# Optimization experiments

Measured on AMD Instinct MI355X. Metric: run time of the kernel, lower is better.

The kernel has to match this reference:

```python
import jax, jax.numpy as jnp
import numpy as np

B, S, H, NH = 2, 2048, 1024, 16
DH = H // NH
FF = 4 * H
EPS = 1e-5


def setup_inputs() -> dict:
    key = jax.random.key(0)
    ks = jax.random.split(key, 16)
    sd = 0.02
    inp = {
        "x": jax.random.normal(ks[0], (B, S, H), dtype=jnp.float32),
        "Wq": jax.random.normal(ks[1], (H, H), dtype=jnp.float32) * sd,
        "bq": jnp.zeros((H,), jnp.float32),
        "Wk": jax.random.normal(ks[2], (H, H), dtype=jnp.float32) * sd,
        "bk": jnp.zeros((H,), jnp.float32),
        "Wv": jax.random.normal(ks[3], (H, H), dtype=jnp.float32) * sd,
        "bv": jnp.zeros((H,), jnp.float32),
        "Wo": jax.random.normal(ks[4], (H, H), dtype=jnp.float32) * sd,
        "bo": jnp.zeros((H,), jnp.float32),
        "W1": jax.random.normal(ks[5], (H, FF), dtype=jnp.float32) * sd,
        "b1": jnp.zeros((FF,), jnp.float32),
        "W2": jax.random.normal(ks[6], (FF, H), dtype=jnp.float32) * sd,
        "b2": jnp.zeros((H,), jnp.float32),
        "g1": jnp.ones((H,), jnp.float32),
        "be1": jnp.zeros((H,), jnp.float32),
        "g2": jnp.ones((H,), jnp.float32),
        "be2": jnp.zeros((H,), jnp.float32),
    }
    return inp


def _layernorm(x, g, b):
    mu = jnp.mean(x, axis=-1, keepdims=True)
    var = jnp.mean(jnp.square(x - mu), axis=-1, keepdims=True)
    return (x - mu) * jax.lax.rsqrt(var + EPS) * g + b


def _block(x, Wq, bq, Wk, bk, Wv, bv, Wo, bo, W1, b1, W2, b2, g1, be1, g2, be2):
    # pre-LN attention
    h = _layernorm(x, g1, be1)
    q = (h @ Wq + bq).reshape(B, S, NH, DH)
    k = (h @ Wk + bk).reshape(B, S, NH, DH)
    v = (h @ Wv + bv).reshape(B, S, NH, DH)
    scale = DH ** -0.5
    scores = jnp.einsum("bqhd,bkhd->bhqk", q, k) * scale  # [B,NH,S,S]
    causal = jnp.tril(jnp.ones((S, S), dtype=bool))
    scores = jnp.where(causal, scores, -jnp.inf)
    attn = jax.nn.softmax(scores, axis=-1)
    out = jnp.einsum("bhqk,bkhd->bqhd", attn, v).reshape(B, S, H)
    x = x + (out @ Wo + bo)
    # pre-LN FFN with exact GELU (torch nn.GELU default)
    h = _layernorm(x, g2, be2)
    h = jax.nn.gelu(h @ W1 + b1, approximate=False)
    return x + (h @ W2 + b2)


def reference(x, Wq, bq, Wk, bk, Wv, bv, Wo, bo, W1, b1, W2, b2, g1, be1, g2, be2):
    return _block(x, Wq, bq, Wk, bk, Wv, bv, Wo, bo, W1, b1, W2, b2, g1, be1, g2, be2)
```

## Files before the change

kernel.cpp:

```cpp
#include <hip/hip_runtime.h>
#include <cstdint>
#include <cstddef>

typedef unsigned short u16;
typedef __attribute__((ext_vector_type(8))) __bf16 bf16v8;
typedef __attribute__((ext_vector_type(8))) unsigned short u16x8;
typedef __attribute__((ext_vector_type(4))) float f32x4;

constexpr int Bc = 2, Sc = 2048, Hc = 1024, NHc = 16, DHc = 64, FFc = 4096;
constexpr int Mc = Bc * Sc;

__device__ __forceinline__ u16 f2bf(float f) {
  unsigned u = __builtin_bit_cast(unsigned, f);
  return (u16)((u + 0x7FFFu + ((u >> 16) & 1u)) >> 16);
}

__device__ __forceinline__ int xcd_swz(int bid, int n) {
  const int q = n >> 3;
  return (bid & 7) * q + (bid >> 3);
}

__device__ __forceinline__ void gload_lds16(const void* g, void* l) {
  __builtin_amdgcn_global_load_lds(
      (const __attribute__((address_space(1))) unsigned*)(uintptr_t)g,
      (__attribute__((address_space(3))) unsigned*)(unsigned)(uintptr_t)l,
      16, 0, 0);
}

struct WP6 { const float* wq; const float* wk; const float* wv; const float* wo;
             const float* w1; const float* w2; };
__global__ __launch_bounds__(256) void wconv_all_kernel(WP6 p, u16* __restrict__ wqkv,
                                                        u16* __restrict__ d1,
                                                        u16* __restrict__ d2) {
  __shared__ float tile[64][65];
  const int z = blockIdx.z;
  const int bid = blockIdx.x;
  const float* W;
  u16* dst;
  int K, N;
  if (z < 4) {
    if (bid >= 256) return;
    W = (z == 0) ? p.wq : (z == 1) ? p.wk : (z == 2) ? p.wv : p.wo;
    dst = wqkv + ((size_t)z << 20);
    K = 1024; N = 1024;
  } else if (z == 4) {
    W = p.w1; dst = d1; K = 1024; N = 4096;
  } else {
    W = p.w2; dst = d2; K = 4096; N = 1024;
  }
  const int nb = N >> 6;
  const int n0 = (bid % nb) << 6, k0 = (bid / nb) << 6;
  const int t = threadIdx.x;
  const int col = t & 63, r0 = t >> 6;
#pragma unroll
  for (int i = 0; i < 16; ++i) {
    int r = (i << 2) + r0;
    tile[r][col] = W[(size_t)(k0 + r) * N + n0 + col];
  }
  __syncthreads();
#pragma unroll
  for (int i = 0; i < 16; ++i) {
    int n = (i << 2) + r0;
    dst[(size_t)(n0 + n) * K + k0 + col] = f2bf(tile[col][n]);
  }
}

__global__ __launch_bounds__(256) void ln_kernel(const float* __restrict__ x,
                                                 const float* __restrict__ g,
                                                 const float* __restrict__ be,
                                                 u16* __restrict__ y) {
  const int row = blockIdx.x;
  const int t = threadIdx.x;
  const float4 v = ((const float4*)(x + (size_t)row * Hc))[t];
  float s1 = v.x + v.y + v.z + v.w;
  float s2 = v.x * v.x + v.y * v.y + v.z * v.z + v.w * v.w;
#pragma unroll
  for (int o = 32; o > 0; o >>= 1) {
    s1 += __shfl_xor(s1, o);
    s2 += __shfl_xor(s2, o);
  }
  __shared__ float r1[4], r2[4];
  const int wave = t >> 6, lane = t & 63;
  if (lane == 0) { r1[wave] = s1; r2[wave] = s2; }
  __syncthreads();
  s1 = r1[0] + r1[1] + r1[2] + r1[3];
  s2 = r2[0] + r2[1] + r2[2] + r2[3];
  const float mu = s1 * (1.f / Hc);
  const float var = s2 * (1.f / Hc) - mu * mu;
  const float rs = rsqrtf(var + 1e-5f);
  const float4 gv = ((const float4*)g)[t];
  const float4 bv = ((const float4*)be)[t];
  ushort4 ov;
  ov.x = f2bf((v.x - mu) * rs * gv.x + bv.x);
  ov.y = f2bf((v.y - mu) * rs * gv.y + bv.y);
  ov.z = f2bf((v.z - mu) * rs * gv.z + bv.z);
  ov.w = f2bf((v.w - mu) * rs * gv.w + bv.w);
  ((ushort4*)(y + (size_t)row * Hc))[t] = ov;
}

template <int EPI>
__global__ __launch_bounds__(256, 2) void gemm_kernel(
    const u16* __restrict__ A, const u16* __restrict__ Bt,
    const float* __restrict__ bias, const float* __restrict__ res,
    u16* __restrict__ outb, float* __restrict__ outf,
    int N, int Kext, int lda, int ldb, int nx) {
  __shared__ __align__(16) char smraw[32768];
  u16 (*As)[128][32] = (u16(*)[128][32])smraw;
  u16 (*Bs)[128][32] = (u16(*)[128][32])(smraw + 16384);
  float (*Cs)[16][132] = (float(*)[16][132])smraw;

  const int t = threadIdx.x;
  const int wave = t >> 6, lane = t & 63;
  const int pid = xcd_swz(blockIdx.x, gridDim.x);
  const int bn = pid % nx, bm = pid / nx;
  const int wm = wave >> 1, wn = wave & 1;
  const int fr = lane & 15, fk = (lane >> 4) << 3;

  f32x4 acc[4][4] = {};

  const int srow = (wave << 4) + (lane >> 2);
  const int scol = (lane & 3) << 3;
  const u16* Ag0 = A + (size_t)(bm * 128 + srow) * lda + scol;
  const u16* Ag1 = Ag0 + (size_t)64 * lda;
  const u16* Bg0 = Bt + (size_t)(bn * 128 + srow) * ldb + scol;
  const u16* Bg1 = Bg0 + (size_t)64 * ldb;

  const int nk = Kext >> 5;
  auto STAGE = [&](int buf, int k0) {
    gload_lds16(Ag0 + k0, &As[buf][wave << 4][0]);
    gload_lds16(Ag1 + k0, &As[buf][64 + (wave << 4)][0]);
    gload_lds16(Bg0 + k0, &Bs[buf][wave << 4][0]);
    gload_lds16(Bg1 + k0, &Bs[buf][64 + (wave << 4)][0]);
  };

  STAGE(0, 0);
  int cur = 0;
  for (int kt = 0; kt < nk; ++kt) {
    if (kt + 1 < nk) {
      STAGE(cur ^ 1, (kt + 1) << 5);
      asm volatile("s_waitcnt vmcnt(4)" ::: "memory");
    } else {
      asm volatile("s_waitcnt vmcnt(0)" ::: "memory");
    }
    __builtin_amdgcn_s_barrier();
    bf16v8 af[4], bfr[4];
#pragma unroll
    for (int i = 0; i < 4; ++i) af[i] = *(const bf16v8*)&As[cur][(wm << 6) + (i << 4) + fr][fk];
#pragma unroll
    for (int j = 0; j < 4; ++j) bfr[j] = *(const bf16v8*)&Bs[cur][(wn << 6) + (j << 4) + fr][fk];
    asm volatile("s_waitcnt lgkmcnt(0)" ::: "memory");
    __builtin_amdgcn_s_barrier();
    __builtin_amdgcn_s_setprio(1);
#pragma unroll
    for (int i = 0; i < 4; ++i)
#pragma unroll
      for (int j = 0; j < 4; ++j)
        acc[i][j] = __builtin_amdgcn_mfma_f32_16x16x32_bf16(af[i], bfr[j], acc[i][j], 0, 0, 0);
    __builtin_amdgcn_s_setprio(0);
    cur ^= 1;
  }
  __syncthreads();

  const int cr = (lane >> 4) << 2, cc = lane & 15;
  const int b2 = t >> 7, u = t & 127, lr = u >> 3, c0 = (u & 7) << 4;

  for (int i = 0; i < 4; ++i) {
#pragma unroll
    for (int j = 0; j < 4; ++j) {
      int col = (wn << 6) + (j << 4) + cc;
      float bz = bias[(bn << 7) + col];
#pragma unroll
      for (int r = 0; r < 4; ++r) Cs[wm][cr + r][col] = acc[i][j][r] + bz;
    }
    __syncthreads();
    {
      const float* crow = &Cs[b2][lr][c0];
      f32x4 v0 = *(const f32x4*)(crow);
      f32x4 v1 = *(const f32x4*)(crow + 4);
      f32x4 v2 = *(const f32x4*)(crow + 8);
      f32x4 v3 = *(const f32x4*)(crow + 12);
      const int grow = (bm << 7) + (b2 << 6) + (i << 4) + lr;
      const int gc = (bn << 7) + c0;
      const size_t base = (size_t)grow * N + gc;
      if constexpr (EPI == 0 || EPI == 1) {
        float vv[16];
#pragma unroll
        for (int k = 0; k < 4; ++k) { vv[k] = v0[k]; vv[4 + k] = v1[k]; vv[8 + k] = v2[k]; vv[12 + k] = v3[k]; }
        if constexpr (EPI == 1) {
#pragma unroll
          for (int k = 0; k < 16; ++k)
            vv[k] = 0.5f * vv[k] * (1.0f + erff(vv[k] * 0.70710678118654752f));
        }
        u16x8 o0, o1;
#pragma unroll
        for (int k = 0; k < 8; ++k) { o0[k] = f2bf(vv[k]); o1[k] = f2bf(vv[8 + k]); }
        *(u16x8*)&outb[base] = o0;
        *(u16x8*)&outb[base + 8] = o1;
      } else {
        const f32x4* rp = (const f32x4*)&res[base];
        v0 += rp[0]; v1 += rp[1]; v2 += rp[2]; v3 += rp[3];
        f32x4* op = (f32x4*)&outf[base];
        op[0] = v0; op[1] = v1; op[2] = v2; op[3] = v3;
      }
    }
    __syncthreads();
  }
}

template <int EPI>
__global__ __launch_bounds__(256, 2) void gemm_p_kernel(
    const u16* __restrict__ A, const u16* __restrict__ Bt,
    const float* __restrict__ bias, const float* __restrict__ res,
    u16* __restrict__ outb, float* __restrict__ outf,
    int N, int Kext, int lda, int ldb, int nx) {
  __shared__ __align__(16) char smraw[49152];
  u16 (*As)[128][32] = (u16(*)[128][32])smraw;
  u16 (*Bs)[128][32] = (u16(*)[128][32])(smraw + 24576);
  float (*Cs)[16][132] = (float(*)[16][132])smraw;

  const int t = threadIdx.x;
  const int wave = t >> 6, lane = t & 63;
  const int pid = xcd_swz(blockIdx.x, gridDim.x);
  const int bn = pid % nx, bm = pid / nx;
  const int wm = wave >> 1, wn = wave & 1;
  const int fr = lane & 15, fk = (lane >> 4) << 3;

  f32x4 acc[4][4] = {};

  const int srow = (wave << 4) + (lane >> 2);
  const int scol = (lane & 3) << 3;
  const u16* Ag0 = A + (size_t)(bm * 128 + srow) * lda + scol;
  const u16* Ag1 = Ag0 + (size_t)64 * lda;
  const u16* Bg0 = Bt + (size_t)(bn * 128 + srow) * ldb + scol;
  const u16* Bg1 = Bg0 + (size_t)64 * ldb;

  const int nk = Kext >> 5;
  auto STAGE = [&](int buf, int k0) {
    gload_lds16(Ag0 + k0, &As[buf][wave << 4][0]);
    gload_lds16(Ag1 + k0, &As[buf][64 + (wave << 4)][0]);
    gload_lds16(Bg0 + k0, &Bs[buf][wave << 4][0]);
    gload_lds16(Bg1 + k0, &Bs[buf][64 + (wave << 4)][0]);
  };

  STAGE(0, 0);
  STAGE(1, 32);
  int cur = 0;
  for (int kt = 0; kt < nk; ++kt) {
    if (kt + 2 < nk) {
      int sb = cur + 2; if (sb >= 3) sb -= 3;
      STAGE(sb, (kt + 2) << 5);
      asm volatile("s_waitcnt vmcnt(8)" ::: "memory");
    } else if (kt + 1 < nk) {
      asm volatile("s_waitcnt vmcnt(4)" ::: "memory");
    } else {
      asm volatile("s_waitcnt vmcnt(0)" ::: "memory");
    }
    __builtin_amdgcn_s_barrier();
    bf16v8 af[4], bfr[4];
#pragma unroll
    for (int i = 0; i < 4; ++i) af[i] = *(const bf16v8*)&As[cur][(wm << 6) + (i << 4) + fr][fk];
#pragma unroll
    for (int j = 0; j < 4; ++j) bfr[j] = *(const bf16v8*)&Bs[cur][(wn << 6) + (j << 4) + fr][fk];
    asm volatile("s_waitcnt lgkmcnt(0)" ::: "memory");
    __builtin_amdgcn_s_barrier();
    __builtin_amdgcn_s_setprio(1);
#pragma unroll
    for (int i = 0; i < 4; ++i)
#pragma unroll
      for (int j = 0; j < 4; ++j)
        acc[i][j] = __builtin_amdgcn_mfma_f32_16x16x32_bf16(af[i], bfr[j], acc[i][j], 0, 0, 0);
    __builtin_amdgcn_s_setprio(0);
    cur = (cur + 1 == 3) ? 0 : cur + 1;
  }
  __syncthreads();

  const int cr = (lane >> 4) << 2, cc = lane & 15;
  const int b2 = t >> 7, u = t & 127, lr = u >> 3, c0 = (u & 7) << 4;

  for (int i = 0; i < 4; ++i) {
#pragma unroll
    for (int j = 0; j < 4; ++j) {
      int col = (wn << 6) + (j << 4) + cc;
      float bz = bias[(bn << 7) + col];
#pragma unroll
      for (int r = 0; r < 4; ++r) Cs[wm][cr + r][col] = acc[i][j][r] + bz;
    }
    __syncthreads();
    {
      const float* crow = &Cs[b2][lr][c0];
      f32x4 v0 = *(const f32x4*)(crow);
      f32x4 v1 = *(const f32x4*)(crow + 4);
      f32x4 v2 = *(const f32x4*)(crow + 8);
      f32x4 v3 = *(const f32x4*)(crow + 12);
      const int grow = (bm << 7) + (b2 << 6) + (i << 4) + lr;
      const int gc = (bn << 7) + c0;
      const size_t base = (size_t)grow * N + gc;
      if constexpr (EPI == 0 || EPI == 1) {
        float vv[16];
#pragma unroll
        for (int k = 0; k < 4; ++k) { vv[k] = v0[k]; vv[4 + k] = v1[k]; vv[8 + k] = v2[k]; vv[12 + k] = v3[k]; }
        if constexpr (EPI == 1) {
#pragma unroll
          for (int k = 0; k < 16; ++k)
            vv[k] = 0.5f * vv[k] * (1.0f + erff(vv[k] * 0.70710678118654752f));
        }
        u16x8 o0, o1;
#pragma unroll
        for (int k = 0; k < 8; ++k) { o0[k] = f2bf(vv[k]); o1[k] = f2bf(vv[8 + k]); }
        *(u16x8*)&outb[base] = o0;
        *(u16x8*)&outb[base + 8] = o1;
      } else {
        const f32x4* rp = (const f32x4*)&res[base];
        v0 += rp[0]; v1 += rp[1]; v2 += rp[2]; v3 += rp[3];
        f32x4* op = (f32x4*)&outf[base];
        op[0] = v0; op[1] = v1; op[2] = v2; op[3] = v3;
      }
    }
    __syncthreads();
  }
}

__global__ __launch_bounds__(256, 2) void qkv_gemm_kernel(
    const u16* __restrict__ A, const u16* __restrict__ Bt,
    const float* __restrict__ bq, const float* __restrict__ bk,
    const float* __restrict__ bv,
    u16* __restrict__ Qb, u16* __restrict__ Kb, u16* __restrict__ Vtg) {
  constexpr int K = 1024;
  __shared__ __align__(16) char smraw[49152];
  u16 (*As)[128][32] = (u16(*)[128][32])smraw;
  u16 (*Bs)[128][32] = (u16(*)[128][32])(smraw + 24576);
  float (*Cs)[16][132] = (float(*)[16][132])smraw;

  const int t = threadIdx.x;
  const int wave = t >> 6, lane = t & 63;
  const int pid = xcd_swz(blockIdx.x, 768);
  const int bn = pid % 24, bm = pid / 24;
  const int wm = wave >> 1, wn = wave & 1;
  const int fr = lane & 15, fk = (lane >> 4) << 3;
  const int seg = bn >> 3;

  f32x4 acc[4][4] = {};

  const int srow = (wave << 4) + (lane >> 2);
  const int scol = (lane & 3) << 3;
  const u16* Ag0 = A + (size_t)(bm * 128 + srow) * K + scol;
  const u16* Ag1 = Ag0 + (size_t)64 * K;
  const u16* Bg0 = Bt + (size_t)(bn * 128 + srow) * K + scol;
  const u16* Bg1 = Bg0 + (size_t)64 * K;

  const int nk = K >> 5;
  auto STAGE = [&](int buf, int k0) {
    gload_lds16(Ag0 + k0, &As[buf][wave << 4][0]);
    gload_lds16(Ag1 + k0, &As[buf][64 + (wave << 4)][0]);
    gload_lds16(Bg0 + k0, &Bs[buf][wave << 4][0]);
    gload_lds16(Bg1 + k0, &Bs[buf][64 + (wave << 4)][0]);
  };

  STAGE(0, 0);
  STAGE(1, 32);
  int cur = 0;
  for (int kt = 0; kt < nk; ++kt) {
    if (kt + 2 < nk) {
      int sb = cur + 2; if (sb >= 3) sb -= 3;
      STAGE(sb, (kt + 2) << 5);
      asm volatile("s_waitcnt vmcnt(8)" ::: "memory");
    } else if (kt + 1 < nk) {
      asm volatile("s_waitcnt vmcnt(4)" ::: "memory");
    } else {
      asm volatile("s_waitcnt vmcnt(0)" ::: "memory");
    }
    __builtin_amdgcn_s_barrier();
    bf16v8 af[4], bfr[4];
#pragma unroll
    for (int i = 0; i < 4; ++i) af[i] = *(const bf16v8*)&As[cur][(wm << 6) + (i << 4) + fr][fk];
#pragma unroll
    for (int j = 0; j < 4; ++j) bfr[j] = *(const bf16v8*)&Bs[cur][(wn << 6) + (j << 4) + fr][fk];
    asm volatile("s_waitcnt lgkmcnt(0)" ::: "memory");
    __builtin_amdgcn_s_barrier();
    __builtin_amdgcn_s_setprio(1);
#pragma unroll
    for (int i = 0; i < 4; ++i)
#pragma unroll
      for (int j = 0; j < 4; ++j)
        acc[i][j] = __builtin_amdgcn_mfma_f32_16x16x32_bf16(af[i], bfr[j], acc[i][j], 0, 0, 0);
    __builtin_amdgcn_s_setprio(0);
    cur = (cur + 1 == 3) ? 0 : cur + 1;
  }
  __syncthreads();

  const int cr = (lane >> 4) << 2, cc = lane & 15;
  const int b2 = t >> 7, u = t & 127, lr = u >> 3, c0 = (u & 7) << 4;
  const float* bp = (seg == 0) ? bq : (seg == 1) ? bk : bv;

  for (int i = 0; i < 4; ++i) {
#pragma unroll
    for (int j = 0; j < 4; ++j) {
      int col = (wn << 6) + (j << 4) + cc;
      float bz = bp[((bn << 7) + col) & 1023];
#pragma unroll
      for (int r = 0; r < 4; ++r) Cs[wm][cr + r][col] = acc[i][j][r] + bz;
    }
    __syncthreads();
    if (seg < 2) {
      const float* crow = &Cs[b2][lr][c0];
      f32x4 v0 = *(const f32x4*)(crow);
      f32x4 v1 = *(const f32x4*)(crow + 4);
      f32x4 v2 = *(const f32x4*)(crow + 8);
      f32x4 v3 = *(const f32x4*)(crow + 12);
      const int grow = (bm << 7) + (b2 << 6) + (i << 4) + lr;
      const int cn0 = (((bn & 7) << 7) + c0);
      u16* dst = (seg == 0) ? Qb : Kb;
      u16x8 o0, o1;
#pragma unroll
      for (int k = 0; k < 4; ++k) {
        o0[k] = f2bf(v0[k]); o0[4 + k] = f2bf(v1[k]);
        o1[k] = f2bf(v2[k]); o1[4 + k] = f2bf(v3[k]);
      }
      *(u16x8*)&dst[(size_t)grow * 1024 + cn0] = o0;
      *(u16x8*)&dst[(size_t)grow * 1024 + cn0 + 8] = o1;
    } else {
      const int cv = ((bn & 7) << 7) + u;
      const int h = cv >> 6, dh = cv & 63;
#pragma unroll
      for (int oct = 0; oct < 2; ++oct) {
        u16x8 o;
#pragma unroll
        for (int k = 0; k < 8; ++k) o[k] = f2bf(Cs[b2][(oct << 3) + k][u]);
        const int srow2 = (bm << 7) + (b2 << 6) + (i << 4) + (oct << 3);
        const int bb = srow2 >> 11, s = srow2 & 2047;
        size_t idx = ((size_t)(bb * 16 + h)) * (64 * 2048) + (size_t)dh * 2048 + s;
        *(u16x8*)&Vtg[idx] = o;
      }
    }
    __syncthreads();
  }
}

__global__ __launch_bounds__(512, 2) void attn_kernel(const u16* __restrict__ Q,
                                                      const u16* __restrict__ Kb,
                                                      const u16* __restrict__ Vt,
                                                      u16* __restrict__ O) {
  constexpr float CS = 0.18033688011112042f;
  constexpr float M2 = 8.0f;
  const int pid = xcd_swz(blockIdx.x, 256);
  const int bx = pid & 7, bh = pid >> 3;
  const int t = threadIdx.x, wave = t >> 6, lane = t & 63;
  const int fr = lane & 15, fk = (lane >> 4) << 3;

  __shared__ u16 Ks[2][64][72];
  __shared__ u16 Vs[2][64][72];
  __shared__ u16 Ps[8][16][72];

  const size_t base = ((size_t)(bh >> 4) * Sc) * Hc + (bh & 15) * DHc;
  const u16* Qp = Q + base;
  const u16* Kp = Kb + base;
  const u16* Vp = Vt + (size_t)bh * (64 * 2048);

  const int r_st = t >> 3;
  const int co_st = (t & 7) << 3;

  bf16v8 ones;
#pragma unroll
  for (int k = 0; k < 8; ++k) ones[k] = (__bf16)1.0f;

  for (int half = 0; half < 2; ++half) {
    const int QT = half ? (15 - bx) : bx;
    const int q0 = QT << 7;
    const int nt = (QT + 1) << 1;

    const int qrow = q0 + (wave << 4) + fr;
    const bf16v8 qf0 = *(const bf16v8*)&Qp[(size_t)qrow * Hc + fk];
    const bf16v8 qf1 = *(const bf16v8*)&Qp[(size_t)qrow * Hc + 32 + fk];

    f32x4 oacc[4] = {};
    f32x4 osum = {};

    const int crow0 = q0 + (wave << 4) + ((lane >> 4) << 2);

    u16x8 rk, rv;
    auto LD = [&](int kv0) {
      rk = *(const u16x8*)&Kp[(size_t)(kv0 + r_st) * Hc + co_st];
      rv = *(const u16x8*)&Vp[(size_t)r_st * 2048 + kv0 + co_st];
    };
    auto WR = [&](int buf) {
      *(u16x8*)&Ks[buf][r_st][co_st] = rk;
      *(u16x8*)&Vs[buf][r_st][co_st] = rv;
    };

    LD(0);
    WR(0);
    __syncthreads();
    int cur = 0;
    for (int it = 0; it < nt; ++it) {
      const int kv0 = it << 6;
      const bool hasnext = (it + 1 < nt);
      if (hasnext) LD(kv0 + 64);

      f32x4 sc[4];
      __builtin_amdgcn_s_setprio(1);
#pragma unroll
      for (int c = 0; c < 4; ++c) {
        bf16v8 kf0 = *(const bf16v8*)&Ks[cur][(c << 4) + fr][fk];
        bf16v8 kf1 = *(const bf16v8*)&Ks[cur][(c << 4) + fr][32 + fk];
        f32x4 a = {0.f, 0.f, 0.f, 0.f};
        a = __builtin_amdgcn_mfma_f32_16x16x32_bf16(qf0, kf0, a, 0, 0, 0);
        a = __builtin_amdgcn_mfma_f32_16x16x32_bf16(qf1, kf1, a, 0, 0, 0);
        sc[c] = a;
      }
      __builtin_amdgcn_s_setprio(0);

      if (kv0 + 64 > q0) {
#pragma unroll
        for (int c = 0; c < 4; ++c)
#pragma unroll
          for (int r = 0; r < 4; ++r) {
            int kv = kv0 + (c << 4) + fr;
            if (kv > crow0 + r) sc[c][r] = -INFINITY;
          }
      }

#pragma unroll
      for (int c = 0; c < 4; ++c)
#pragma unroll
        for (int r = 0; r < 4; ++r) {
          float p = exp2f(fmaf(sc[c][r], CS, -M2));
          Ps[wave][((lane >> 4) << 2) + r][(c << 4) + fr] = f2bf(p);
        }

      const bf16v8 pa0 = *(const bf16v8*)&Ps[wave][fr][fk];
      const bf16v8 pa1 = *(const bf16v8*)&Ps[wave][fr][32 + fk];
      __builtin_amdgcn_s_setprio(1);
#pragma unroll
      for (int f = 0; f < 4; ++f) {
        bf16v8 vf0 = *(const bf16v8*)&Vs[cur][(f << 4) + fr][fk];
        bf16v8 vf1 = *(const bf16v8*)&Vs[cur][(f << 4) + fr][32 + fk];
        oacc[f] = __builtin_amdgcn_mfma_f32_16x16x32_bf16(pa0, vf0, oacc[f], 0, 0, 0);
        oacc[f] = __builtin_amdgcn_mfma_f32_16x16x32_bf16(pa1, vf1, oacc[f], 0, 0, 0);
      }
      osum = __builtin_amdgcn_mfma_f32_16x16x32_bf16(pa0, ones, osum, 0, 0, 0);
      osum = __builtin_amdgcn_mfma_f32_16x16x32_bf16(pa1, ones, osum, 0, 0, 0);
      __builtin_amdgcn_s_setprio(0);

      if (hasnext) WR(cur ^ 1);
      __syncthreads();
      cur ^= 1;
    }
#pragma unroll
    for (int r = 0; r < 4; ++r) {
      float inv = 1.0f / osum[r];
      int row = crow0 + r;
#pragma unroll
      for (int f = 0; f < 4; ++f)
        O[base + (size_t)row * Hc + (f << 4) + fr] = f2bf(oacc[f][r] * inv);
    }
    __syncthreads();
  }
}

extern "C" void kernel_launch(void* const* d_in, const int* in_sizes, int n_in,
                              void* d_out, int out_size, void* d_ws, size_t ws_size,
                              hipStream_t stream) {
  const float* x  = (const float*)d_in[0];
  const float* Wq = (const float*)d_in[1];
  const float* bq = (const float*)d_in[2];
  const float* Wk = (const float*)d_in[3];
  const float* bk = (const float*)d_in[4];
  const float* Wv = (const float*)d_in[5];
  const float* bv = (const float*)d_in[6];
  const float* Wo = (const float*)d_in[7];
  const float* bo = (const float*)d_in[8];
  const float* W1 = (const float*)d_in[9];
  const float* b1 = (const float*)d_in[10];
  const float* W2 = (const float*)d_in[11];
  const float* b2 = (const float*)d_in[12];
  const float* g1 = (const float*)d_in[13];
  const float* be1 = (const float*)d_in[14];
  const float* g2 = (const float*)d_in[15];
  const float* be2 = (const float*)d_in[16];
  float* out = (float*)d_out;

  char* ws = (char*)d_ws;
  const size_t MB = 1024 * 1024;
  u16* wqkv = (u16*)(ws + 0 * MB);
  u16* wo   = (u16*)(ws + 6 * MB);
  u16* w1   = (u16*)(ws + 8 * MB);
  u16* w2   = (u16*)(ws + 16 * MB);
  u16* lnb  = (u16*)(ws + 24 * MB);
  u16* Qb   = (u16*)(ws + 32 * MB);
  u16* Kb   = (u16*)(ws + 40 * MB);
  u16* Vtg  = (u16*)(ws + 48 * MB);
  u16* Ob   = (u16*)(ws + 56 * MB);
  u16* H1   = (u16*)(ws + 32 * MB);

  dim3 blk(256);
  WP6 wp{Wq, Wk, Wv, Wo, W1, W2};
  wconv_all_kernel<<<dim3(1024, 1, 6), blk, 0, stream>>>(wp, wqkv, w1, w2);

  ln_kernel<<<Mc, blk, 0, stream>>>(x, g1, be1, lnb);

  qkv_gemm_kernel<<<dim3(768), blk, 0, stream>>>(lnb, wqkv, bq, bk, bv, Qb, Kb, Vtg);

  attn_kernel<<<dim3(256), dim3(512), 0, stream>>>(Qb, Kb, Vtg, Ob);

  gemm_p_kernel<2><<<dim3(256), blk, 0, stream>>>(Ob, wo, bo, x, nullptr, out,
                                                  1024, 1024, 1024, 1024, 8);

  ln_kernel<<<Mc, blk, 0, stream>>>(out, g2, be2, lnb);

  gemm_kernel<1><<<dim3(1024), blk, 0, stream>>>(lnb, w1, b1, nullptr, H1, nullptr,
                                                 4096, 1024, 1024, 1024, 32);

  gemm_p_kernel<2><<<dim3(256), blk, 0, stream>>>(H1, w2, b2, out, nullptr, out,
                                                  1024, 4096, 4096, 4096, 8);
}
```

Before: 241.8 us.

## Use double-buffered QKV GEMM staging and two-deep register prefetch in attention

The QKV GEMM drops from a three-stage to a two-stage LDS pipeline, cutting shared memory from 48KB to 32KB per block. That should allow more resident blocks, at the cost of less load latency hiding. The attention loop is unrolled by two with alternating register sets (A/B), so K/V tiles are prefetched from global memory two iterations ahead. The number of KV tiles is always even, so the unroll by two covers every tile.

```diff
diff --git a/kernel.cpp b/kernel.cpp
--- a/kernel.cpp
+++ b/kernel.cpp
@@ -326,9 +326,9 @@
     const float* __restrict__ bv,
     u16* __restrict__ Qb, u16* __restrict__ Kb, u16* __restrict__ Vtg) {
   constexpr int K = 1024;
-  __shared__ __align__(16) char smraw[49152];
+  __shared__ __align__(16) char smraw[32768];
   u16 (*As)[128][32] = (u16(*)[128][32])smraw;
-  u16 (*Bs)[128][32] = (u16(*)[128][32])(smraw + 24576);
+  u16 (*Bs)[128][32] = (u16(*)[128][32])(smraw + 16384);
   float (*Cs)[16][132] = (float(*)[16][132])smraw;
 
   const int t = threadIdx.x;
@@ -357,14 +357,10 @@
   };
 
   STAGE(0, 0);
-  STAGE(1, 32);
   int cur = 0;
   for (int kt = 0; kt < nk; ++kt) {
-    if (kt + 2 < nk) {
-      int sb = cur + 2; if (sb >= 3) sb -= 3;
-      STAGE(sb, (kt + 2) << 5);
-      asm volatile("s_waitcnt vmcnt(8)" ::: "memory");
-    } else if (kt + 1 < nk) {
+    if (kt + 1 < nk) {
+      STAGE(cur ^ 1, (kt + 1) << 5);
       asm volatile("s_waitcnt vmcnt(4)" ::: "memory");
     } else {
       asm volatile("s_waitcnt vmcnt(0)" ::: "memory");
@@ -384,7 +380,7 @@
       for (int j = 0; j < 4; ++j)
         acc[i][j] = __builtin_amdgcn_mfma_f32_16x16x32_bf16(af[i], bfr[j], acc[i][j], 0, 0, 0);
     __builtin_amdgcn_s_setprio(0);
-    cur = (cur + 1 == 3) ? 0 : cur + 1;
+    cur ^= 1;
   }
   __syncthreads();
 
@@ -477,38 +473,36 @@
 
     const int crow0 = q0 + (wave << 4) + ((lane >> 4) << 2);
 
-    u16x8 rk, rv;
-    auto LD = [&](int kv0) {
-      rk = *(const u16x8*)&Kp[(size_t)(kv0 + r_st) * Hc + co_st];
-      rv = *(const u16x8*)&Vp[(size_t)r_st * 2048 + kv0 + co_st];
+    u16x8 rkA, rvA, rkB, rvB;
+    auto LDA = [&](int kv0) {
+      rkA = *(const u16x8*)&Kp[(size_t)(kv0 + r_st) * Hc + co_st];
+      rvA = *(const u16x8*)&Vp[(size_t)r_st * 2048 + kv0 + co_st];
     };
-    auto WR = [&](int buf) {
-      *(u16x8*)&Ks[buf][r_st][co_st] = rk;
-      *(u16x8*)&Vs[buf][r_st][co_st] = rv;
+    auto LDB = [&](int kv0) {
+      rkB = *(const u16x8*)&Kp[(size_t)(kv0 + r_st) * Hc + co_st];
+      rvB = *(const u16x8*)&Vp[(size_t)r_st * 2048 + kv0 + co_st];
     };
-
-    LD(0);
-    WR(0);
-    __syncthreads();
-    int cur = 0;
-    for (int it = 0; it < nt; ++it) {
-      const int kv0 = it << 6;
-      const bool hasnext = (it + 1 < nt);
-      if (hasnext) LD(kv0 + 64);
-
+    auto WRA = [&](int buf) {
+      *(u16x8*)&Ks[buf][r_st][co_st] = rkA;
+      *(u16x8*)&Vs[buf][r_st][co_st] = rvA;
+    };
+    auto WRB = [&](int buf) {
+      *(u16x8*)&Ks[buf][r_st][co_st] = rkB;
+      *(u16x8*)&Vs[buf][r_st][co_st] = rvB;
+    };
+    auto COMPUTE = [&](int buf, int kv0) {
       f32x4 sc[4];
       __builtin_amdgcn_s_setprio(1);
 #pragma unroll
       for (int c = 0; c < 4; ++c) {
-        bf16v8 kf0 = *(const bf16v8*)&Ks[cur][(c << 4) + fr][fk];
-        bf16v8 kf1 = *(const bf16v8*)&Ks[cur][(c << 4) + fr][32 + fk];
+        bf16v8 kf0 = *(const bf16v8*)&Ks[buf][(c << 4) + fr][fk];
+        bf16v8 kf1 = *(const bf16v8*)&Ks[buf][(c << 4) + fr][32 + fk];
         f32x4 a = {0.f, 0.f, 0.f, 0.f};
         a = __builtin_amdgcn_mfma_f32_16x16x32_bf16(qf0, kf0, a, 0, 0, 0);
         a = __builtin_amdgcn_mfma_f32_16x16x32_bf16(qf1, kf1, a, 0, 0, 0);
         sc[c] = a;
       }
       __builtin_amdgcn_s_setprio(0);
-
       if (kv0 + 64 > q0) {
 #pragma unroll
         for (int c = 0; c < 4; ++c)
@@ -518,7 +512,6 @@
             if (kv > crow0 + r) sc[c][r] = -INFINITY;
           }
       }
-
 #pragma unroll
       for (int c = 0; c < 4; ++c)
 #pragma unroll
@@ -526,24 +519,35 @@
           float p = exp2f(fmaf(sc[c][r], CS, -M2));
           Ps[wave][((lane >> 4) << 2) + r][(c << 4) + fr] = f2bf(p);
         }
-
       const bf16v8 pa0 = *(const bf16v8*)&Ps[wave][fr][fk];
       const bf16v8 pa1 = *(const bf16v8*)&Ps[wave][fr][32 + fk];
       __builtin_amdgcn_s_setprio(1);
 #pragma unroll
       for (int f = 0; f < 4; ++f) {
-        bf16v8 vf0 = *(const bf16v8*)&Vs[cur][(f << 4) + fr][fk];
-        bf16v8 vf1 = *(const bf16v8*)&Vs[cur][(f << 4) + fr][32 + fk];
+        bf16v8 vf0 = *(const bf16v8*)&Vs[buf][(f << 4) + fr][fk];
+        bf16v8 vf1 = *(const bf16v8*)&Vs[buf][(f << 4) + fr][32 + fk];
         oacc[f] = __builtin_amdgcn_mfma_f32_16x16x32_bf16(pa0, vf0, oacc[f], 0, 0, 0);
         oacc[f] = __builtin_amdgcn_mfma_f32_16x16x32_bf16(pa1, vf1, oacc[f], 0, 0, 0);
       }
       osum = __builtin_amdgcn_mfma_f32_16x16x32_bf16(pa0, ones, osum, 0, 0, 0);
       osum = __builtin_amdgcn_mfma_f32_16x16x32_bf16(pa1, ones, osum, 0, 0, 0);
       __builtin_amdgcn_s_setprio(0);
-
-      if (hasnext) WR(cur ^ 1);
+    };
+
+    LDA(0);
+    WRA(0);
+    LDB(64);
+    __syncthreads();
+    for (int it = 0; it < nt; it += 2) {
+      const int kv0 = it << 6;
+      if (it + 2 < nt) LDA(kv0 + 128);
+      COMPUTE(0, kv0);
+      WRB(1);
       __syncthreads();
-      cur ^= 1;
+      if (it + 3 < nt) LDB(kv0 + 192);
+      COMPUTE(1, kv0 + 64);
+      if (it + 2 < nt) WRA(0);
+      __syncthreads();
     }
 #pragma unroll
     for (int r = 0; r < 4; ++r) {
```

New measurement: 244.4 us. No clear change (+1.1%).

## Use 256x256 tiles with swizzled LDS for the FFN up-projection GEMM

Applied to the files above, without the earlier changes.

Replaces the 128x128, 256-thread GEMM for the W1 projection with a 256x256 tile kernel using 512 threads, BK=64 and 128KB of double-buffered LDS. An XOR swizzle on the LDS column index is meant to avoid bank conflicts on fragment reads. The larger tile raises arithmetic intensity and cuts global and LDS traffic per FLOP. In exchange it runs only one block per CU, 256 blocks in total, and needs more accumulator registers, so latency hiding and wave-tail balance may suffer.

```diff
diff --git a/kernel.cpp b/kernel.cpp
--- a/kernel.cpp
+++ b/kernel.cpp
@@ -99,109 +99,110 @@
 }
 
 template <int EPI>
-__global__ __launch_bounds__(256, 2) void gemm_kernel(
+__global__ __launch_bounds__(512, 1) void gemm256_kernel(
     const u16* __restrict__ A, const u16* __restrict__ Bt,
-    const float* __restrict__ bias, const float* __restrict__ res,
-    u16* __restrict__ outb, float* __restrict__ outf,
-    int N, int Kext, int lda, int ldb, int nx) {
-  __shared__ __align__(16) char smraw[32768];
-  u16 (*As)[128][32] = (u16(*)[128][32])smraw;
-  u16 (*Bs)[128][32] = (u16(*)[128][32])(smraw + 16384);
-  float (*Cs)[16][132] = (float(*)[16][132])smraw;
+    const float* __restrict__ bias, u16* __restrict__ outb,
+    int N, int K, int lda, int ldb, int nx) {
+  __shared__ __align__(16) char smraw[131072];
+  u16 (*As)[256][64] = (u16(*)[256][64])smraw;
+  u16 (*Bs)[256][64] = (u16(*)[256][64])(smraw + 65536);
+  float (*Cs)[260] = (float(*)[260])smraw;
 
   const int t = threadIdx.x;
-  const int wave = t >> 6, lane = t & 63;
+  const int w = t >> 6, l = t & 63;
   const int pid = xcd_swz(blockIdx.x, gridDim.x);
   const int bn = pid % nx, bm = pid / nx;
-  const int wm = wave >> 1, wn = wave & 1;
-  const int fr = lane & 15, fk = (lane >> 4) << 3;
-
-  f32x4 acc[4][4] = {};
-
-  const int srow = (wave << 4) + (lane >> 2);
-  const int scol = (lane & 3) << 3;
-  const u16* Ag0 = A + (size_t)(bm * 128 + srow) * lda + scol;
-  const u16* Ag1 = Ag0 + (size_t)64 * lda;
-  const u16* Bg0 = Bt + (size_t)(bn * 128 + srow) * ldb + scol;
-  const u16* Bg1 = Bg0 + (size_t)64 * ldb;
-
-  const int nk = Kext >> 5;
+  const int wr = w >> 2, wn = w & 3;
+  const int fr = l & 15, fk = (l >> 4) << 3;
+  const int fs = (fr & 7) << 3;
+
+  f32x4 acc[8][4] = {};
+
+  const int srow = (w << 3) + (l >> 3);
+  const int scol = (((l & 7) ^ ((l >> 3) & 7)) << 3);
+  const u16* Ag = A + (size_t)(bm * 256 + srow) * lda + scol;
+  const u16* Bg = Bt + (size_t)(bn * 256 + srow) * ldb + scol;
+
   auto STAGE = [&](int buf, int k0) {
-    gload_lds16(Ag0 + k0, &As[buf][wave << 4][0]);
-    gload_lds16(Ag1 + k0, &As[buf][64 + (wave << 4)][0]);
-    gload_lds16(Bg0 + k0, &Bs[buf][wave << 4][0]);
-    gload_lds16(Bg1 + k0, &Bs[buf][64 + (wave << 4)][0]);
+#pragma unroll
+    for (int i = 0; i < 4; ++i)
+      gload_lds16(Ag + (size_t)(i << 6) * lda + k0,
+                  smraw + (buf << 15) + (i << 13) + (w << 10));
+#pragma unroll
+    for (int i = 0; i < 4; ++i)
+      gload_lds16(Bg + (size_t)(i << 6) * ldb + k0,
+                  smraw + 65536 + (buf << 15) + (i << 13) + (w << 10));
   };
 
+  const int nk = K >> 6;
   STAGE(0, 0);
   int cur = 0;
   for (int kt = 0; kt < nk; ++kt) {
     if (kt + 1 < nk) {
-      STAGE(cur ^ 1, (kt + 1) << 5);
-      asm volatile("s_waitcnt vmcnt(4)" ::: "memory");
+      STAGE(cur ^ 1, (kt + 1) << 6);
+      asm volatile("s_waitcnt vmcnt(8)" ::: "memory");
     } else {
       asm volatile("s_waitcnt vmcnt(0)" ::: "memory");
     }
     __builtin_amdgcn_s_barrier();
-    bf16v8 af[4], bfr[4];
-#pragma unroll
-    for (int i = 0; i < 4; ++i) af[i] = *(const bf16v8*)&As[cur][(wm << 6) + (i << 4) + fr][fk];
-#pragma unroll
-    for (int j = 0; j < 4; ++j) bfr[j] = *(const bf16v8*)&Bs[cur][(wn << 6) + (j << 4) + fr][fk];
+    bf16v8 bfr[4][2], af[8][2];
+#pragma unroll
+    for (int nj = 0; nj < 4; ++nj) {
+      const u16* brow = &Bs[cur][(wn << 6) + (nj << 4) + fr][0];
+#pragma unroll
+      for (int kh = 0; kh < 2; ++kh)
+        bfr[nj][kh] = *(const bf16v8*)&brow[((kh << 5) + fk) ^ fs];
+    }
+#pragma unroll
+    for (int mi = 0; mi < 8; ++mi) {
+      const u16* arow = &As[cur][(wr << 7) + (mi << 4) + fr][0];
+      af[mi][0] = *(const bf16v8*)&arow[fk ^ fs];
+      af[mi][1] = *(const bf16v8*)&arow[(32 + fk) ^ fs];
+    }
     asm volatile("s_waitcnt lgkmcnt(0)" ::: "memory");
     __builtin_amdgcn_s_barrier();
     __builtin_amdgcn_s_setprio(1);
 #pragma unroll
-    for (int i = 0; i < 4; ++i)
-#pragma unroll
-      for (int j = 0; j < 4; ++j)
-        acc[i][j] = __builtin_amdgcn_mfma_f32_16x16x32_bf16(af[i], bfr[j], acc[i][j], 0, 0, 0);
+    for (int mi = 0; mi < 8; ++mi)
+#pragma unroll
+      for (int nj = 0; nj < 4; ++nj) {
+        acc[mi][nj] = __builtin_amdgcn_mfma_f32_16x16x32_bf16(af[mi][0], bfr[nj][0], acc[mi][nj], 0, 0, 0);
+        acc[mi][nj] = __builtin_amdgcn_mfma_f32_16x16x32_bf16(af[mi][1], bfr[nj][1], acc[mi][nj], 0, 0, 0);
+      }
     __builtin_amdgcn_s_setprio(0);
     cur ^= 1;
   }
   __syncthreads();
 
-  const int cr = (lane >> 4) << 2, cc = lane & 15;
-  const int b2 = t >> 7, u = t & 127, lr = u >> 3, c0 = (u & 7) << 4;
-
-  for (int i = 0; i < 4; ++i) {
-#pragma unroll
-    for (int j = 0; j < 4; ++j) {
-      int col = (wn << 6) + (j << 4) + cc;
-      float bz = bias[(bn << 7) + col];
-#pragma unroll
-      for (int r = 0; r < 4; ++r) Cs[wm][cr + r][col] = acc[i][j][r] + bz;
+  const int cr = (l >> 4) << 2, cc = l & 15;
+  const int row32 = t >> 4, col16 = (t & 15) << 4;
+#pragma unroll
+  for (int mi = 0; mi < 8; ++mi) {
+#pragma unroll
+    for (int nj = 0; nj < 4; ++nj) {
+      const int col = (wn << 6) + (nj << 4) + cc;
+      const float bz = bias[(bn << 8) + col];
+#pragma unroll
+      for (int r = 0; r < 4; ++r) Cs[(wr << 4) + cr + r][col] = acc[mi][nj][r] + bz;
     }
     __syncthreads();
     {
-      const float* crow = &Cs[b2][lr][c0];
-      f32x4 v0 = *(const f32x4*)(crow);
-      f32x4 v1 = *(const f32x4*)(crow + 4);
-      f32x4 v2 = *(const f32x4*)(crow + 8);
-      f32x4 v3 = *(const f32x4*)(crow + 12);
-      const int grow = (bm << 7) + (b2 << 6) + (i << 4) + lr;
-      const int gc = (bn << 7) + c0;
-      const size_t base = (size_t)grow * N + gc;
-      if constexpr (EPI == 0 || EPI == 1) {
-        float vv[16];
-#pragma unroll
-        for (int k = 0; k < 4; ++k) { vv[k] = v0[k]; vv[4 + k] = v1[k]; vv[8 + k] = v2[k]; vv[12 + k] = v3[k]; }
-        if constexpr (EPI == 1) {
-#pragma unroll
-          for (int k = 0; k < 16; ++k)
-            vv[k] = 0.5f * vv[k] * (1.0f + erff(vv[k] * 0.70710678118654752f));
-        }
-        u16x8 o0, o1;
-#pragma unroll
-        for (int k = 0; k < 8; ++k) { o0[k] = f2bf(vv[k]); o1[k] = f2bf(vv[8 + k]); }
-        *(u16x8*)&outb[base] = o0;
-        *(u16x8*)&outb[base + 8] = o1;
-      } else {
-        const f32x4* rp = (const f32x4*)&res[base];
-        v0 += rp[0]; v1 += rp[1]; v2 += rp[2]; v3 += rp[3];
-        f32x4* op = (f32x4*)&outf[base];
-        op[0] = v0; op[1] = v1; op[2] = v2; op[3] = v3;
-      }
+      const float* crow = &Cs[row32][col16];
+      float vv[16];
+#pragma unroll
+      for (int k = 0; k < 16; ++k) vv[k] = crow[k];
+      if constexpr (EPI == 1) {
+#pragma unroll
+        for (int k = 0; k < 16; ++k)
+          vv[k] = 0.5f * vv[k] * (1.0f + erff(vv[k] * 0.70710678118654752f));
+      }
+      u16x8 o0, o1;
+#pragma unroll
+      for (int k = 0; k < 8; ++k) { o0[k] = f2bf(vv[k]); o1[k] = f2bf(vv[8 + k]); }
+      const int grow = (bm << 8) + ((row32 >> 4) << 7) + (mi << 4) + (row32 & 15);
+      const size_t base = (size_t)grow * N + (bn << 8) + col16;
+      *(u16x8*)&outb[base] = o0;
+      *(u16x8*)&outb[base + 8] = o1;
     }
     __syncthreads();
   }
@@ -607,8 +608,8 @@
 
   ln_kernel<<<Mc, blk, 0, stream>>>(out, g2, be2, lnb);
 
-  gemm_kernel<1><<<dim3(1024), blk, 0, stream>>>(lnb, w1, b1, nullptr, H1, nullptr,
-                                                 4096, 1024, 1024, 1024, 32);
+  gemm256_kernel<1><<<dim3(256), dim3(512), 0, stream>>>(lnb, w1, b1, H1,
+                                                         4096, 1024, 1024, 1024, 16);
 
   gemm_p_kernel<2><<<dim3(256), blk, 0, stream>>>(H1, w2, b2, out, nullptr, out,
                                                   1024, 4096, 4096, 4096, 8);
```

Measured after the change: 276.3 us. +14.3%, slower.
